# Kernel optimization log

Hardware: AMD Instinct MI355X
Metric: run time of the kernel (lower is better)

Reference implementation:

```python
import jax, jax.numpy as jnp
import numpy as np

CNN_DIM = 256
CLASS_NUM = 6
NHOPS = 2
ATT_DIM = 50


def conv1d(x, w, b, pad):
    # x: [B, Cin, L], w: [Cout, Cin, K]
    y = jax.lax.conv_general_dilated(x, w, (1,), [(pad, pad)],
                                     dimension_numbers=('NCH', 'OIH', 'NCH'))
    return y + b[None, :, None]


def setup_inputs() -> dict:
    key = jax.random.key(0)
    ks = jax.random.split(key, 16)
    B, L, V, GE, DE = 8, 128, 30000, 300, 100
    IN = GE + DE
    C = CLASS_NUM
    s = 0.02
    inp = {}
    inp['x'] = jax.random.randint(ks[0], (B, L), 0, V)
    inp['x_len'] = L  # python int, stands in for x_len[0] (max length)
    inp['x_mask'] = jnp.ones((B, L), dtype=jnp.float32)
    inp['gen_table'] = jax.random.normal(ks[1], (V, GE), jnp.float32) * s
    inp['domain_table'] = jax.random.normal(ks[2], (V, DE), jnp.float32) * s
    inp['w1'] = jax.random.normal(ks[3], (128, IN, 5)) * s
    inp['b1'] = jnp.zeros((128,))
    inp['w2'] = jax.random.normal(ks[4], (128, IN, 3)) * s
    inp['b2'] = jnp.zeros((128,))
    inp['w3'] = jax.random.normal(ks[5], (256, 256, 5)) * s
    inp['b3'] = jnp.zeros((256,))
    inp['w4'] = jax.random.normal(ks[6], (256, 256, 5)) * s
    inp['b4'] = jnp.zeros((256,))
    inp['w5'] = jax.random.normal(ks[7], (256, 256, 5)) * s
    inp['b5'] = jnp.zeros((256,))
    inp['wq'] = jax.random.normal(ks[8], (CNN_DIM, ATT_DIM)) * s
    inp['bq'] = jnp.zeros((ATT_DIM,))
    inp['wv'] = jax.random.normal(ks[9], (CNN_DIM, ATT_DIM)) * s
    inp['bv'] = jnp.zeros((ATT_DIM,))
    inp['vv'] = jax.random.normal(ks[10], (ATT_DIM,)) * s
    inp['wf'] = jax.random.normal(ks[11], (2 * CNN_DIM + 3 * C, 2 * CNN_DIM)) * s
    inp['bf'] = jnp.zeros((2 * CNN_DIM,))
    inp['wc'] = jax.random.normal(ks[12], (2 * CNN_DIM, C)) * s
    inp['bc'] = jnp.zeros((C,))
    return inp


def reference(x, x_len, x_mask, gen_table, domain_table,
              w1, b1, w2, b2, w3, b3, w4, b4, w5, b5,
              wq, bq, wv, bv, vv, wf, bf, wc, bc):
    # embeddings (dropout omitted: eval mode)
    emb = jnp.concatenate([gen_table[x], domain_table[x]], axis=2)  # [B,L,400]
    xe = jnp.swapaxes(emb, 1, 2)  # [B,400,L]
    xc = jax.nn.relu(jnp.concatenate([conv1d(xe, w1, b1, 2),
                                      conv1d(xe, w2, b2, 1)], axis=1))
    xc = jax.nn.relu(conv1d(xc, w3, b3, 2))
    xc = jax.nn.relu(conv1d(xc, w4, b4, 2))
    xc = jax.nn.relu(conv1d(xc, w5, b5, 2))
    xc = jnp.swapaxes(xc, 1, 2)[:, :x_len, :]  # [B,L,256]
    mask = x_mask[:, :x_len]
    # perceptron (additive) self-attention: v^T tanh(Wq q_i + Wv v_j)
    q = xc @ wq + bq  # [B,L,50]
    v = xc @ wv + bv  # [B,L,50]
    scores = jnp.tanh(q[:, :, None, :] + v[:, None, :, :]) @ vv  # [B,L,L]
    scores = jnp.where(mask[:, None, :] == 0, -1e9, scores)
    attn = jax.nn.softmax(scores, axis=2)
    merged = jnp.einsum('bij,bjd->bid', attn, xc) * mask[:, :, None]
    xc = xc + merged
    B, L, D = xc.shape
    # grid features: (i,j) -> [h_i, h_j]
    features = jnp.concatenate([
        jnp.broadcast_to(xc[:, :, None, :], (B, L, L, D)),
        jnp.broadcast_to(xc[:, None, :, :], (B, L, L, D))], axis=3)  # [B,L,L,512]
    # upper-triangular validity mask on the grid
    m2 = jnp.triu(mask[:, None, :] * mask[:, :, None])[..., None]  # [B,L,L,1]
    logits = features @ wc + bc  # [B,L,L,C]
    for _ in range(NHOPS):
        probs = logits
        lg = probs * m2
        lm = jnp.maximum(jnp.max(lg, axis=1), jnp.max(lg, axis=2))  # [B,L,C]
        row = jnp.broadcast_to(lm[:, :, None, :], (B, L, L, lm.shape[-1]))
        grid = jnp.concatenate([row, jnp.swapaxes(row, 1, 2)], axis=3)  # [B,L,L,2C]
        features = jnp.concatenate([features, grid, probs], axis=3) @ wf + bf
        logits = features @ wc + bc
    return logits
```

## Files before the change

### kernel.cpp

```cpp
#include <hip/hip_runtime.h>
#include <math.h>

#define LSEQ 128
#define BB 8
#define M_TOK (BB*LSEQ)

typedef __attribute__((ext_vector_type(8))) short short8;
typedef __attribute__((ext_vector_type(4))) float floatx4;

__device__ __forceinline__ unsigned short bf16_rne(float v) {
    union { float f; unsigned u; } a; a.f = v;
    return (unsigned short)((a.u + 0x7fffu + ((a.u >> 16) & 1u)) >> 16);
}
__device__ __forceinline__ float bf16_to_f(unsigned short h) {
    union { unsigned u; float f; } b; b.u = ((unsigned)h) << 16;
    return b.f;
}
__device__ __forceinline__ void split2(float v, unsigned short& h, unsigned short& l) {
    h = bf16_rne(v);
    l = bf16_rne(v - bf16_to_f(h));
}

struct PreArgs {
    const float *w1, *w2, *w3, *w4, *w5;
    unsigned short *B1h, *B1l, *B2h, *B2l, *B3h, *B3l, *B4h, *B4l, *B5h, *B5l;
    const int* x;
    const float* gen;
    const float* dom;
    unsigned short *Eh, *El;
    const float* wf;
    const float* wc;
    float* Wfc;
};
__global__ __launch_bounds__(256) void stage_kernel(PreArgs a) {
    int y = blockIdx.y;
    int tid = threadIdx.x;
    if (y < 3) {
        const float* w = (y == 0) ? a.w3 : (y == 1) ? a.w4 : a.w5;
        unsigned short* dh = (y == 0) ? a.B3h : (y == 1) ? a.B4h : a.B5h;
        unsigned short* dl = (y == 0) ? a.B3l : (y == 1) ? a.B4l : a.B5l;
        int idx = blockIdx.x * 256 + tid;
        int j = idx & 7;
        int n = (idx >> 3) & 255;
        int g = idx >> 11;
        int cg = g & 31, kk = g >> 5;
        int ci = cg * 8 + j;
        float v = w[(n * 256 + ci) * 5 + kk];
        unsigned short h, l; split2(v, h, l);
        dh[idx] = h; dl[idx] = l;
    } else if (y == 3) {
        int idx = blockIdx.x * 256 + tid;
        if (idx >= 5 * 52 * 128 * 8) return;
        int j = idx & 7;
        int n = (idx >> 3) & 127;
        int g = idx >> 10;
        int cg = g % 52, kk = g / 52;
        int ci = cg * 8 + j;
        float v = (ci < 400) ? a.w1[(n * 400 + ci) * 5 + kk] : 0.f;
        unsigned short h, l; split2(v, h, l);
        a.B1h[idx] = h; a.B1l[idx] = l;
    } else if (y == 4) {
        int idx = blockIdx.x * 256 + tid;
        if (idx >= 3 * 52 * 128 * 8) return;
        int j = idx & 7;
        int n = (idx >> 3) & 127;
        int g = idx >> 10;
        int cg = g % 52, kk = g / 52;
        int ci = cg * 8 + j;
        float v = (ci < 400) ? a.w2[(n * 400 + ci) * 3 + kk] : 0.f;
        unsigned short h, l; split2(v, h, l);
        a.B2h[idx] = h; a.B2l[idx] = l;
    } else if (y == 5) {
        int m = blockIdx.x;
        if (m >= M_TOK) return;
        int t = a.x[m];
        for (int c = tid; c < 416; c += 256) {
            float v = (c < 300) ? a.gen[t * 300 + c]
                    : (c < 400) ? a.dom[t * 100 + (c - 300)] : 0.f;
            unsigned short h, l; split2(v, h, l);
            a.Eh[m * 416 + c] = h;
            a.El[m * 416 + c] = l;
        }
    } else {
        int r = blockIdx.x;
        if (r >= 512 || tid >= 64) return;
        int l = tid;
        float p[6] = {0,0,0,0,0,0};
        const float* row = a.wf + r * 512;
        #pragma unroll
        for (int k = 0; k < 8; ++k) {
            int n = l + 64 * k;
            float v = row[n];
            #pragma unroll
            for (int c = 0; c < 6; ++c) p[c] += v * a.wc[n * 6 + c];
        }
        #pragma unroll
        for (int c = 0; c < 6; ++c)
            for (int off = 32; off >= 1; off >>= 1) p[c] += __shfl_xor(p[c], off, 64);
        if (l == 0) {
            #pragma unroll
            for (int c = 0; c < 6; ++c) a.Wfc[r * 6 + c] = p[c];
        }
    }
}

__global__ __launch_bounds__(256) void conv1_mfma(
        const unsigned short* __restrict__ Eh, const unsigned short* __restrict__ El,
        const unsigned short* __restrict__ B1h, const unsigned short* __restrict__ B1l,
        const unsigned short* __restrict__ B2h, const unsigned short* __restrict__ B2l,
        const float* __restrict__ b1, const float* __restrict__ b2,
        unsigned short* __restrict__ Xoh, unsigned short* __restrict__ Xol,
        const float* __restrict__ wf, const float* __restrict__ bf,
        const float* __restrict__ wc, const float* __restrict__ Wfc,
        float* __restrict__ U) {
    __shared__ __align__(16) unsigned short xsh[20 * 424];
    __shared__ __align__(16) unsigned short xsl[20 * 424];
    int by = blockIdx.y;
    int tid = threadIdx.x;
    if (by == 4) {
        if (tid >= 64) return;
        int l = tid;
        for (int i = 0; i < 9; ++i) {
            int r = blockIdx.x + 64 * i;
            if (r >= 531) break;
            const float* row = (r < 530) ? (wf + r * 512) : bf;
            float p[12];
            #pragma unroll
            for (int c = 0; c < 12; ++c) p[c] = 0.f;
            #pragma unroll
            for (int k = 0; k < 8; ++k) {
                int n = l + 64 * k;
                float v = row[n];
                #pragma unroll
                for (int c = 0; c < 6; ++c) {
                    p[c]     += v * wc[n * 6 + c];
                    p[c + 6] += v * Wfc[n * 6 + c];
                }
            }
            #pragma unroll
            for (int c = 0; c < 12; ++c)
                for (int off = 32; off >= 1; off >>= 1) p[c] += __shfl_xor(p[c], off, 64);
            if (l == 0) {
                #pragma unroll
                for (int c = 0; c < 12; ++c) U[r * 12 + c] = p[c];
            }
        }
        return;
    }
    int mt = blockIdx.x;
    int p0 = mt * 16;
    int b = p0 >> 7, l0 = p0 & 127;
    for (int i = tid; i < 2 * 1040; i += 256) {
        int sel = i >= 1040;
        int u2 = sel ? i - 1040 : i;
        int j = u2 / 52, cg = u2 % 52;
        int l = l0 - 2 + j;
        short8 v = {0,0,0,0,0,0,0,0};
        if (l >= 0 && l < 128) {
            const unsigned short* src = (sel ? El : Eh) + (b * 128 + l) * 416 + cg * 8;
            v = *(const short8*)src;
        }
        *(short8*)((sel ? xsl : xsh) + j * 424 + cg * 8) = v;
    }
    __syncthreads();
    int w = tid >> 6, lane = tid & 63;
    int m = lane & 15, q = lane >> 4;
    bool br2 = (by >= 2);
    int n0b = (by & 1) * 64;
    int nB = n0b + w * 16 + m;
    floatx4 acc0 = {0,0,0,0}, acc1 = {0,0,0,0}, acc2 = {0,0,0,0};
    if (!br2) {
        for (int kk = 0; kk < 5; ++kk) {
            const unsigned short* arh = xsh + (m + kk) * 424;
            const unsigned short* arl = xsl + (m + kk) * 424;
            #pragma unroll
            for (int u = 0; u < 13; ++u) {
                short8 ah = *(const short8*)(arh + u * 32 + q * 8);
                short8 al = *(const short8*)(arl + u * 32 + q * 8);
                int boff = (((kk * 52 + u * 4 + q) * 128) + nB) * 8;
                short8 bh = *(const short8*)(B1h + boff);
                short8 bl = *(const short8*)(B1l + boff);
                acc0 = __builtin_amdgcn_mfma_f32_16x16x32_bf16(ah, bh, acc0, 0, 0, 0);
                acc1 = __builtin_amdgcn_mfma_f32_16x16x32_bf16(ah, bl, acc1, 0, 0, 0);
                acc2 = __builtin_amdgcn_mfma_f32_16x16x32_bf16(al, bh, acc2, 0, 0, 0);
            }
        }
    } else {
        for (int kk = 0; kk < 3; ++kk) {
            const unsigned short* arh = xsh + (m + kk + 1) * 424;
            const unsigned short* arl = xsl + (m + kk + 1) * 424;
            #pragma unroll
            for (int u = 0; u < 13; ++u) {
                short8 ah = *(const short8*)(arh + u * 32 + q * 8);
                short8 al = *(const short8*)(arl + u * 32 + q * 8);
                int boff = (((kk * 52 + u * 4 + q) * 128) + nB) * 8;
                short8 bh = *(const short8*)(B2h + boff);
                short8 bl = *(const short8*)(B2l + boff);
                acc0 = __builtin_amdgcn_mfma_f32_16x16x32_bf16(ah, bh, acc0, 0, 0, 0);
                acc1 = __builtin_amdgcn_mfma_f32_16x16x32_bf16(ah, bl, acc1, 0, 0, 0);
                acc2 = __builtin_amdgcn_mfma_f32_16x16x32_bf16(al, bh, acc2, 0, 0, 0);
            }
        }
    }
    __syncthreads();
    float* fl = (float*)xsh;
    #pragma unroll
    for (int reg = 0; reg < 4; ++reg)
        fl[(q * 4 + reg) * 68 + w * 16 + m] = acc0[reg] + acc1[reg] + acc2[reg];
    __syncthreads();
    int ocb = br2 ? 128 + n0b : n0b;
    const float* bias = br2 ? b2 : b1;
    #pragma unroll
    for (int i = 0; i < 4; ++i) {
        int e = tid + 256 * i;
        int mm = e >> 6, nn = e & 63;
        float val = fl[mm * 68 + nn] + bias[n0b + nn];
        val = fmaxf(val, 0.f);
        unsigned short h, l; split2(val, h, l);
        int o = (p0 + mm) * 256 + ocb + nn;
        Xoh[o] = h; Xol[o] = l;
    }
}

__global__ __launch_bounds__(256) void conv256_mfma(
        const unsigned short* __restrict__ Xih, const unsigned short* __restrict__ Xil,
        const unsigned short* __restrict__ Bh, const unsigned short* __restrict__ Bl,
        const float* __restrict__ bias, int outmode,
        unsigned short* __restrict__ Xoh, unsigned short* __restrict__ Xol,
        float* __restrict__ fout) {
    __shared__ __align__(16) unsigned short xsh[36 * 264];
    __shared__ __align__(16) unsigned short xsl[36 * 264];
    int mt = blockIdx.x;
    int p0 = mt * 32;
    int b = p0 >> 7, l0 = p0 & 127;
    int n0 = blockIdx.y * 64;
    int tid = threadIdx.x;
    for (int i = tid; i < 2 * 1152; i += 256) {
        int sel = i >= 1152;
        int u2 = sel ? i - 1152 : i;
        int j = u2 >> 5, cg = u2 & 31;
        int l = l0 - 2 + j;
        short8 v = {0,0,0,0,0,0,0,0};
        if (l >= 0 && l < 128) {
            const unsigned short* src = (sel ? Xil : Xih) + (b * 128 + l) * 256 + cg * 8;
            v = *(const short8*)src;
        }
        *(short8*)((sel ? xsl : xsh) + j * 264 + cg * 8) = v;
    }
    __syncthreads();
    int w = tid >> 6, lane = tid & 63;
    int m = lane & 15, q = lane >> 4;
    int nB = n0 + w * 16 + m;
    floatx4 acc0a = {0,0,0,0}, acc1a = {0,0,0,0}, acc2a = {0,0,0,0};
    floatx4 acc0b = {0,0,0,0}, acc1b = {0,0,0,0}, acc2b = {0,0,0,0};
    for (int kk = 0; kk < 5; ++kk) {
        const unsigned short* arh0 = xsh + (m + kk) * 264;
        const unsigned short* arl0 = xsl + (m + kk) * 264;
        const unsigned short* arh1 = arh0 + 16 * 264;
        const unsigned short* arl1 = arl0 + 16 * 264;
        #pragma unroll
        for (int u = 0; u < 8; ++u) {
            short8 ah0 = *(const short8*)(arh0 + u * 32 + q * 8);
            short8 al0 = *(const short8*)(arl0 + u * 32 + q * 8);
            short8 ah1 = *(const short8*)(arh1 + u * 32 + q * 8);
            short8 al1 = *(const short8*)(arl1 + u * 32 + q * 8);
            int boff = (((kk * 32 + u * 4 + q) * 256) + nB) * 8;
            short8 bh = *(const short8*)(Bh + boff);
            short8 bl = *(const short8*)(Bl + boff);
            acc0a = __builtin_amdgcn_mfma_f32_16x16x32_bf16(ah0, bh, acc0a, 0, 0, 0);
            acc1a = __builtin_amdgcn_mfma_f32_16x16x32_bf16(ah0, bl, acc1a, 0, 0, 0);
            acc2a = __builtin_amdgcn_mfma_f32_16x16x32_bf16(al0, bh, acc2a, 0, 0, 0);
            acc0b = __builtin_amdgcn_mfma_f32_16x16x32_bf16(ah1, bh, acc0b, 0, 0, 0);
            acc1b = __builtin_amdgcn_mfma_f32_16x16x32_bf16(ah1, bl, acc1b, 0, 0, 0);
            acc2b = __builtin_amdgcn_mfma_f32_16x16x32_bf16(al1, bh, acc2b, 0, 0, 0);
        }
    }
    __syncthreads();
    float* fl = (float*)xsh;
    #pragma unroll
    for (int reg = 0; reg < 4; ++reg) {
        fl[(q * 4 + reg) * 68 + w * 16 + m]        = acc0a[reg] + acc1a[reg] + acc2a[reg];
        fl[(16 + q * 4 + reg) * 68 + w * 16 + m]   = acc0b[reg] + acc1b[reg] + acc2b[reg];
    }
    __syncthreads();
    #pragma unroll
    for (int i = 0; i < 8; ++i) {
        int e = tid + 256 * i;
        int mm = e >> 6, nn = e & 63;
        float val = fl[mm * 68 + nn] + bias[n0 + nn];
        val = fmaxf(val, 0.f);
        int o = (p0 + mm) * 256 + n0 + nn;
        if (outmode == 0) {
            unsigned short h, l; split2(val, h, l);
            Xoh[o] = h; Xol[o] = l;
        } else {
            fout[o] = val;
        }
    }
}

__global__ __launch_bounds__(128) void qv_v2(const float* __restrict__ xc,
        const float* __restrict__ wq, const float* __restrict__ bq,
        const float* __restrict__ wv, const float* __restrict__ bv,
        float* __restrict__ q, float* __restrict__ v) {
    int m = blockIdx.x;
    int tid = threadIdx.x;
    int w = tid >> 6, d = tid & 63;
    if (d >= 50) return;
    const float* W = w ? wv : wq;
    float a = w ? bv[d] : bq[d];
    const float* xm = xc + m * 256;
    #pragma unroll 8
    for (int c = 0; c < 256; ++c) a += xm[c] * W[c * 50 + d];
    (w ? v : q)[m * 50 + d] = a;
}

__global__ __launch_bounds__(256) void attn_v2(const float* __restrict__ xc,
        const float* __restrict__ q, const float* __restrict__ v,
        const float* __restrict__ vv, const float* __restrict__ xmask,
        const float* __restrict__ wc, const float* __restrict__ bc,
        float* __restrict__ xc2, float* __restrict__ f0, float* __restrict__ g0) {
    __shared__ float vs[128 * 50];
    __shared__ float spart[128], aarr[128], xrow[256], qrow[52], vvs[52], red[4];
    int bi = blockIdx.x;
    int b = bi >> 7;
    int tid = threadIdx.x;
    for (int idx = tid; idx < 128 * 50; idx += 256) vs[idx] = v[b * 6400 + idx];
    if (tid < 50) { qrow[tid] = q[bi * 50 + tid]; vvs[tid] = vv[tid]; }
    __syncthreads();
    int j = tid & 127, half = tid >> 7;
    int d0 = half * 25;
    const float* vj = vs + j * 50 + d0;
    float s = 0.f;
    #pragma unroll
    for (int d = 0; d < 25; ++d) {
        float x = qrow[d0 + d] + vj[d];
        float e = __expf(2.f * x);
        s += (1.f - 2.f / (e + 1.f)) * vvs[d0 + d];
    }
    if (half) spart[j] = s;
    __syncthreads();
    float stot = 0.f;
    if (!half) {
        stot = s + spart[j];
        if (xmask[b * LSEQ + j] == 0.f) stot = -1e9f;
    }
    if (tid < 128) {
        float m = stot;
        #pragma unroll
        for (int off = 32; off >= 1; off >>= 1) m = fmaxf(m, __shfl_xor(m, off, 64));
        if ((tid & 63) == 0) red[tid >> 6] = m;
    }
    __syncthreads();
    float mx = fmaxf(red[0], red[1]);
    float e = 0.f;
    if (tid < 128) {
        e = __expf(stot - mx);
        float su = e;
        #pragma unroll
        for (int off = 32; off >= 1; off >>= 1) su += __shfl_xor(su, off, 64);
        if ((tid & 63) == 0) red[2 + (tid >> 6)] = su;
    }
    __syncthreads();
    float denom = red[2] + red[3];
    if (tid < 128) aarr[j] = e / denom;
    __syncthreads();
    float maskI = xmask[bi];
    const float* xcb = xc + b * LSEQ * 256;
    float acc = 0.f;
    #pragma unroll 8
    for (int jj = 0; jj < 128; ++jj) acc += aarr[jj] * xcb[jj * 256 + tid];
    float val = xc[bi * 256 + tid] + acc * maskI;
    xc2[bi * 256 + tid] = val;
    xrow[tid] = val;
    __syncthreads();
    int grp = tid >> 4, l16 = tid & 15;
    if (grp < 12) {
        int c = grp % 6, gsel = grp / 6;
        const float* wcc = wc + gsel * 256 * 6 + c;
        float a = 0.f;
        #pragma unroll
        for (int ch = l16; ch < 256; ch += 16) a += xrow[ch] * wcc[ch * 6];
        #pragma unroll
        for (int off = 8; off >= 1; off >>= 1) a += __shfl_down(a, off, 16);
        if (l16 == 0) {
            if (gsel == 0) f0[bi * 6 + c] = a + bc[c];
            else           g0[bi * 6 + c] = a;
        }
    }
}

__global__ __launch_bounds__(256) void hop1_kernel(const float* __restrict__ xc2,
        const float* __restrict__ U, const float* __restrict__ f0,
        const float* __restrict__ g0, const float* __restrict__ bc,
        float* __restrict__ outF, float* __restrict__ outG) {
    __shared__ float sf0[768], sg0[768], sfw[768], sgw[768], lms[768];
    int b = blockIdx.x >> 4, grp = blockIdx.x & 15;
    int tid = threadIdx.x;
    for (int i = tid; i < 768; i += 256) {
        sf0[i] = f0[b * 768 + i];
        sg0[i] = g0[b * 768 + i];
    }
    __syncthreads();
    int p = tid;
    float fv[6], gv[6], pf[6], sx[6];
    if (p < 128) {
        #pragma unroll
        for (int c = 0; c < 6; ++c) {
            fv[c] = sf0[p * 6 + c]; gv[c] = sg0[p * 6 + c];
            pf[c] = fv[c]; sx[c] = gv[c];
            sfw[p * 6 + c] = fv[c]; sgw[p * 6 + c] = gv[c];
        }
    }
    __syncthreads();
    #pragma unroll
    for (int off = 1; off < 128; off <<= 1) {
        float av[6], dv[6];
        if (p < 128) {
            #pragma unroll
            for (int c = 0; c < 6; ++c) {
                av[c] = (p >= off) ? sfw[(p - off) * 6 + c] : -INFINITY;
                dv[c] = (p + off < 128) ? sgw[(p + off) * 6 + c] : -INFINITY;
            }
        }
        __syncthreads();
        if (p < 128) {
            #pragma unroll
            for (int c = 0; c < 6; ++c) {
                pf[c] = fmaxf(pf[c], av[c]); sx[c] = fmaxf(sx[c], dv[c]);
                sfw[p * 6 + c] = pf[c]; sgw[p * 6 + c] = sx[c];
            }
        }
        __syncthreads();
    }
    if (p < 128) {
        #pragma unroll
        for (int c = 0; c < 6; ++c) {
            float M1 = pf[c] + gv[c];
            if (p < LSEQ - 1) M1 = fmaxf(M1, 0.f);
            float M2 = fv[c] + sx[c];
            if (p > 0) M2 = fmaxf(M2, 0.f);
            lms[p * 6 + c] = fmaxf(M1, M2);
        }
    }
    __syncthreads();
    int t = tid >> 5, lane = tid & 31;
    int ptok = grp * 8 + t;
    int m = b * 128 + ptok;
    float p24[24];
    #pragma unroll
    for (int c = 0; c < 24; ++c) p24[c] = 0.f;
    const floatx4* U4 = (const floatx4*)U;
    const float* xm = xc2 + m * 256;
    #pragma unroll
    for (int kk = 0; kk < 8; ++kk) {
        int k = lane + 32 * kk;
        float a = xm[k];
        floatx4 u0[3], u1[3];
        #pragma unroll
        for (int t3 = 0; t3 < 3; ++t3) { u0[t3] = U4[k * 3 + t3]; u1[t3] = U4[(256 + k) * 3 + t3]; }
        #pragma unroll
        for (int t3 = 0; t3 < 3; ++t3)
            #pragma unroll
            for (int qd = 0; qd < 4; ++qd) {
                p24[t3 * 4 + qd]      += a * u0[t3][qd];
                p24[12 + t3 * 4 + qd] += a * u1[t3][qd];
            }
    }
    #pragma unroll
    for (int c = 0; c < 24; ++c)
        for (int off = 16; off >= 1; off >>= 1) p24[c] += __shfl_xor(p24[c], off, 32);
    if (lane < 12) {
        int c = lane;
        float s0 = p24[c], s1 = p24[12 + c];
        #pragma unroll
        for (int jj = 0; jj < 6; ++jj) {
            float lmv = lms[ptok * 6 + jj];
            float f0v = sf0[ptok * 6 + jj];
            float g0v = sg0[ptok * 6 + jj];
            float dbv = U[(524 + jj) * 12 + c];
            s0 += lmv * U[(512 + jj) * 12 + c] + f0v * dbv;
            s1 += lmv * U[(518 + jj) * 12 + c] + g0v * dbv;
        }
        s0 += U[530 * 12 + c];
        if (c < 6) s0 += bc[c];
        outF[m * 12 + c] = s0;
        outG[m * 12 + c] = s1;
    }
}

__global__ __launch_bounds__(256) void hop2_kernel(const float* __restrict__ f1phi,
        const float* __restrict__ g1gam, const float* __restrict__ U,
        const float* __restrict__ bc, float* __restrict__ out) {
    __shared__ float f1s[128 * 12], g1s[128 * 12];
    __shared__ float sfw[768], sgw[768], lm1s[768], f2s[768], g2s[768];
    __shared__ float Us[228], bcs[6];
    int b = blockIdx.x >> 4, ys = blockIdx.x & 15;
    int tid = threadIdx.x;
    for (int i = tid; i < 1536; i += 256) {
        f1s[i] = f1phi[b * 1536 + i];
        g1s[i] = g1gam[b * 1536 + i];
    }
    if (tid < 228) Us[tid] = U[512 * 12 + tid];
    if (tid < 6) bcs[tid] = bc[tid];
    __syncthreads();
    int p = tid;
    float fv[6], gv[6], pf[6], sx[6];
    if (p < 128) {
        #pragma unroll
        for (int c = 0; c < 6; ++c) {
            fv[c] = f1s[p * 12 + c]; gv[c] = g1s[p * 12 + c];
            pf[c] = fv[c]; sx[c] = gv[c];
            sfw[p * 6 + c] = fv[c]; sgw[p * 6 + c] = gv[c];
        }
    }
    __syncthreads();
    #pragma unroll
    for (int off = 1; off < 128; off <<= 1) {
        float av[6], dv[6];
        if (p < 128) {
            #pragma unroll
            for (int c = 0; c < 6; ++c) {
                av[c] = (p >= off) ? sfw[(p - off) * 6 + c] : -INFINITY;
                dv[c] = (p + off < 128) ? sgw[(p + off) * 6 + c] : -INFINITY;
            }
        }
        __syncthreads();
        if (p < 128) {
            #pragma unroll
            for (int c = 0; c < 6; ++c) {
                pf[c] = fmaxf(pf[c], av[c]); sx[c] = fmaxf(sx[c], dv[c]);
                sfw[p * 6 + c] = pf[c]; sgw[p * 6 + c] = sx[c];
            }
        }
        __syncthreads();
    }
    if (p < 128) {
        #pragma unroll
        for (int c = 0; c < 6; ++c) {
            float M1 = pf[c] + gv[c];
            if (p < LSEQ - 1) M1 = fmaxf(M1, 0.f);
            float M2 = fv[c] + sx[c];
            if (p > 0) M2 = fmaxf(M2, 0.f);
            lm1s[p * 6 + c] = fmaxf(M1, M2);
        }
    }
    __syncthreads();
    if (p < 128) {
        float lmv[6], f1v[6], g1v[6];
        #pragma unroll
        for (int jj = 0; jj < 6; ++jj) {
            lmv[jj] = lm1s[p * 6 + jj];
            f1v[jj] = f1s[p * 12 + jj];
            g1v[jj] = g1s[p * 12 + jj];
        }
        #pragma unroll
        for (int c = 0; c < 6; ++c) {
            float sf = f1s[p * 12 + 6 + c] + Us[18 * 12 + c] + bcs[c];
            float sg = g1s[p * 12 + 6 + c];
            #pragma unroll
            for (int jj = 0; jj < 6; ++jj) {
                sf += lmv[jj] * Us[jj * 12 + c]       + f1v[jj] * Us[(12 + jj) * 12 + c];
                sg += lmv[jj] * Us[(6 + jj) * 12 + c] + g1v[jj] * Us[(12 + jj) * 12 + c];
            }
            f2s[p * 6 + c] = sf;
            g2s[p * 6 + c] = sg;
        }
    }
    __syncthreads();
    floatx4* out4 = (floatx4*)out;
    for (int e = tid; e < 1536; e += 256) {
        int i = e / 12, part = e - i * 12;
        floatx4 wv;
        #pragma unroll
        for (int qd = 0; qd < 4; ++qd) {
            int idx = part * 4 + qd;
            int jj = idx / 6, c = idx - jj * 6;
            wv[qd] = f2s[i * 6 + c] + g2s[(ys * 8 + jj) * 6 + c];
        }
        out4[(b * 128 + i) * 192 + ys * 12 + part] = wv;
    }
}

extern "C" void kernel_launch(void* const* d_in, const int* in_sizes, int n_in,
                              void* d_out, int out_size, void* d_ws, size_t ws_size,
                              hipStream_t stream) {
    const int*   x     = (const int*)d_in[0];
    const float* xmask = (const float*)d_in[2];
    const float* gen   = (const float*)d_in[3];
    const float* dom   = (const float*)d_in[4];
    const float* w1    = (const float*)d_in[5];
    const float* b1    = (const float*)d_in[6];
    const float* w2    = (const float*)d_in[7];
    const float* b2    = (const float*)d_in[8];
    const float* w3    = (const float*)d_in[9];
    const float* b3    = (const float*)d_in[10];
    const float* w4    = (const float*)d_in[11];
    const float* b4    = (const float*)d_in[12];
    const float* w5    = (const float*)d_in[13];
    const float* b5    = (const float*)d_in[14];
    const float* wq    = (const float*)d_in[15];
    const float* bq    = (const float*)d_in[16];
    const float* wv    = (const float*)d_in[17];
    const float* bv    = (const float*)d_in[18];
    const float* vv    = (const float*)d_in[19];
    const float* wf    = (const float*)d_in[20];
    const float* bf    = (const float*)d_in[21];
    const float* wc    = (const float*)d_in[22];
    const float* bc    = (const float*)d_in[23];

    float* fb = (float*)d_ws;
    float* bufB  = fb;
    float* xc2   = bufB  + 262144;
    float* qb    = xc2   + 262144;
    float* vb    = qb    + 51200;
    float* Wfc   = vb    + 51200;
    float* U     = Wfc   + 3072;
    float* f0    = U     + 6376;
    float* g0    = f0    + 6144;
    float* lm0   = g0    + 6144;
    float* lm1   = lm0   + 6144;
    float* f1phi = lm1   + 6144;
    float* g1gam = f1phi + 12288;
    float* f2    = g1gam + 12288;
    float* g2    = f2    + 6144;
    (void)lm0; (void)lm1; (void)f2;
    unsigned short* sb = (unsigned short*)(g2 + 6144 + 32);
    unsigned short* Eh  = sb;             sb += 425984;
    unsigned short* El  = sb;             sb += 425984;
    unsigned short* B1h = sb;             sb += 266240;
    unsigned short* B1l = sb;             sb += 266240;
    unsigned short* B2h = sb;             sb += 159744;
    unsigned short* B2l = sb;             sb += 159744;
    unsigned short* B3h = sb;             sb += 327680;
    unsigned short* B3l = sb;             sb += 327680;
    unsigned short* B4h = sb;             sb += 327680;
    unsigned short* B4l = sb;             sb += 327680;
    unsigned short* B5h = sb;             sb += 327680;
    unsigned short* B5l = sb;             sb += 327680;
    unsigned short* X3h = sb;             sb += 262144;
    unsigned short* X3l = sb;             sb += 262144;
    unsigned short* X4h = sb;             sb += 262144;
    unsigned short* X4l = sb;             sb += 262144;

    PreArgs pa;
    pa.w1 = w1; pa.w2 = w2; pa.w3 = w3; pa.w4 = w4; pa.w5 = w5;
    pa.B1h = B1h; pa.B1l = B1l; pa.B2h = B2h; pa.B2l = B2l;
    pa.B3h = B3h; pa.B3l = B3l; pa.B4h = B4h; pa.B4l = B4l;
    pa.B5h = B5h; pa.B5l = B5l;
    pa.x = x; pa.gen = gen; pa.dom = dom; pa.Eh = Eh; pa.El = El;
    pa.wf = wf; pa.wc = wc; pa.Wfc = Wfc;
    stage_kernel<<<dim3(1280, 7), 256, 0, stream>>>(pa);

    conv1_mfma<<<dim3(64, 5), 256, 0, stream>>>(Eh, El, B1h, B1l, B2h, B2l, b1, b2,
                                                X3h, X3l, wf, bf, wc, Wfc, U);
    conv256_mfma<<<dim3(32, 4), 256, 0, stream>>>(X3h, X3l, B3h, B3l, b3, 0,
                                                  X4h, X4l, nullptr);
    conv256_mfma<<<dim3(32, 4), 256, 0, stream>>>(X4h, X4l, B4h, B4l, b4, 0,
                                                  X3h, X3l, nullptr);
    conv256_mfma<<<dim3(32, 4), 256, 0, stream>>>(X3h, X3l, B5h, B5l, b5, 1,
                                                  nullptr, nullptr, bufB);

    qv_v2<<<M_TOK, 128, 0, stream>>>(bufB, wq, bq, wv, bv, qb, vb);
    attn_v2<<<M_TOK, 256, 0, stream>>>(bufB, qb, vb, vv, xmask, wc, bc, xc2, f0, g0);

    hop1_kernel<<<128, 256, 0, stream>>>(xc2, U, f0, g0, bc, f1phi, g1gam);
    hop2_kernel<<<128, 256, 0, stream>>>(f1phi, g1gam, U, bc, (float*)d_out);
}
```

Before: 254.9 us.

## Fuse conv layers and q/v projection into one persistent kernel with grid barriers

Merges conv1, the three 256-channel convs and the q/v projection into a single persistent kernel of 320 blocks that synchronise through atomic grid barriers, replacing five separate launches. The conv256 tile shrinks from 32 to 16 rows so 256 blocks cover each layer, which raises parallelism but halves B-operand reuse per block. Barrier counters are zeroed inside stage_kernel. The barriers rely on all 320 blocks being co-resident, and idle blocks spin at every barrier.

```diff
diff --git a/kernel.cpp b/kernel.cpp
--- a/kernel.cpp
+++ b/kernel.cpp
@@ -4,6 +4,7 @@
 #define LSEQ 128
 #define BB 8
 #define M_TOK (BB*LSEQ)
+#define CONV_BLOCKS 320
 
 typedef __attribute__((ext_vector_type(8))) short short8;
 typedef __attribute__((ext_vector_type(4))) float floatx4;
@@ -19,6 +20,18 @@
 __device__ __forceinline__ void split2(float v, unsigned short& h, unsigned short& l) {
     h = bf16_rne(v);
     l = bf16_rne(v - bf16_to_f(h));
+}
+
+__device__ __forceinline__ void gbar(int* bars, int phase, int nb) {
+    __syncthreads();
+    if (threadIdx.x == 0) {
+        __threadfence();
+        __hip_atomic_fetch_add(bars + phase * 64, 1, __ATOMIC_ACQ_REL, __HIP_MEMORY_SCOPE_AGENT);
+        while (__hip_atomic_load(bars + phase * 64, __ATOMIC_ACQUIRE, __HIP_MEMORY_SCOPE_AGENT) < nb)
+            __builtin_amdgcn_s_sleep(2);
+        __threadfence();
+    }
+    __syncthreads();
 }
 
 struct PreArgs {
@@ -31,6 +44,7 @@
     const float* wf;
     const float* wc;
     float* Wfc;
+    int* bars;
 };
 __global__ __launch_bounds__(256) void stage_kernel(PreArgs a) {
     int y = blockIdx.y;
@@ -82,8 +96,12 @@
             a.El[m * 416 + c] = l;
         }
     } else {
+        if (blockIdx.x >= 512) {
+            if (blockIdx.x == 512) a.bars[tid] = 0;
+            return;
+        }
+        if (tid >= 64) return;
         int r = blockIdx.x;
-        if (r >= 512 || tid >= 64) return;
         int l = tid;
         float p[6] = {0,0,0,0,0,0};
         const float* row = a.wf + r * 512;
@@ -104,140 +122,18 @@
     }
 }
 
-__global__ __launch_bounds__(256) void conv1_mfma(
-        const unsigned short* __restrict__ Eh, const unsigned short* __restrict__ El,
-        const unsigned short* __restrict__ B1h, const unsigned short* __restrict__ B1l,
-        const unsigned short* __restrict__ B2h, const unsigned short* __restrict__ B2l,
-        const float* __restrict__ b1, const float* __restrict__ b2,
-        unsigned short* __restrict__ Xoh, unsigned short* __restrict__ Xol,
-        const float* __restrict__ wf, const float* __restrict__ bf,
-        const float* __restrict__ wc, const float* __restrict__ Wfc,
-        float* __restrict__ U) {
-    __shared__ __align__(16) unsigned short xsh[20 * 424];
-    __shared__ __align__(16) unsigned short xsl[20 * 424];
-    int by = blockIdx.y;
-    int tid = threadIdx.x;
-    if (by == 4) {
-        if (tid >= 64) return;
-        int l = tid;
-        for (int i = 0; i < 9; ++i) {
-            int r = blockIdx.x + 64 * i;
-            if (r >= 531) break;
-            const float* row = (r < 530) ? (wf + r * 512) : bf;
-            float p[12];
-            #pragma unroll
-            for (int c = 0; c < 12; ++c) p[c] = 0.f;
-            #pragma unroll
-            for (int k = 0; k < 8; ++k) {
-                int n = l + 64 * k;
-                float v = row[n];
-                #pragma unroll
-                for (int c = 0; c < 6; ++c) {
-                    p[c]     += v * wc[n * 6 + c];
-                    p[c + 6] += v * Wfc[n * 6 + c];
-                }
-            }
-            #pragma unroll
-            for (int c = 0; c < 12; ++c)
-                for (int off = 32; off >= 1; off >>= 1) p[c] += __shfl_xor(p[c], off, 64);
-            if (l == 0) {
-                #pragma unroll
-                for (int c = 0; c < 12; ++c) U[r * 12 + c] = p[c];
-            }
-        }
-        return;
-    }
-    int mt = blockIdx.x;
-    int p0 = mt * 16;
-    int b = p0 >> 7, l0 = p0 & 127;
-    for (int i = tid; i < 2 * 1040; i += 256) {
-        int sel = i >= 1040;
-        int u2 = sel ? i - 1040 : i;
-        int j = u2 / 52, cg = u2 % 52;
-        int l = l0 - 2 + j;
-        short8 v = {0,0,0,0,0,0,0,0};
-        if (l >= 0 && l < 128) {
-            const unsigned short* src = (sel ? El : Eh) + (b * 128 + l) * 416 + cg * 8;
-            v = *(const short8*)src;
-        }
-        *(short8*)((sel ? xsl : xsh) + j * 424 + cg * 8) = v;
-    }
-    __syncthreads();
-    int w = tid >> 6, lane = tid & 63;
-    int m = lane & 15, q = lane >> 4;
-    bool br2 = (by >= 2);
-    int n0b = (by & 1) * 64;
-    int nB = n0b + w * 16 + m;
-    floatx4 acc0 = {0,0,0,0}, acc1 = {0,0,0,0}, acc2 = {0,0,0,0};
-    if (!br2) {
-        for (int kk = 0; kk < 5; ++kk) {
-            const unsigned short* arh = xsh + (m + kk) * 424;
-            const unsigned short* arl = xsl + (m + kk) * 424;
-            #pragma unroll
-            for (int u = 0; u < 13; ++u) {
-                short8 ah = *(const short8*)(arh + u * 32 + q * 8);
-                short8 al = *(const short8*)(arl + u * 32 + q * 8);
-                int boff = (((kk * 52 + u * 4 + q) * 128) + nB) * 8;
-                short8 bh = *(const short8*)(B1h + boff);
-                short8 bl = *(const short8*)(B1l + boff);
-                acc0 = __builtin_amdgcn_mfma_f32_16x16x32_bf16(ah, bh, acc0, 0, 0, 0);
-                acc1 = __builtin_amdgcn_mfma_f32_16x16x32_bf16(ah, bl, acc1, 0, 0, 0);
-                acc2 = __builtin_amdgcn_mfma_f32_16x16x32_bf16(al, bh, acc2, 0, 0, 0);
-            }
-        }
-    } else {
-        for (int kk = 0; kk < 3; ++kk) {
-            const unsigned short* arh = xsh + (m + kk + 1) * 424;
-            const unsigned short* arl = xsl + (m + kk + 1) * 424;
-            #pragma unroll
-            for (int u = 0; u < 13; ++u) {
-                short8 ah = *(const short8*)(arh + u * 32 + q * 8);
-                short8 al = *(const short8*)(arl + u * 32 + q * 8);
-                int boff = (((kk * 52 + u * 4 + q) * 128) + nB) * 8;
-                short8 bh = *(const short8*)(B2h + boff);
-                short8 bl = *(const short8*)(B2l + boff);
-                acc0 = __builtin_amdgcn_mfma_f32_16x16x32_bf16(ah, bh, acc0, 0, 0, 0);
-                acc1 = __builtin_amdgcn_mfma_f32_16x16x32_bf16(ah, bl, acc1, 0, 0, 0);
-                acc2 = __builtin_amdgcn_mfma_f32_16x16x32_bf16(al, bh, acc2, 0, 0, 0);
-            }
-        }
-    }
-    __syncthreads();
-    float* fl = (float*)xsh;
-    #pragma unroll
-    for (int reg = 0; reg < 4; ++reg)
-        fl[(q * 4 + reg) * 68 + w * 16 + m] = acc0[reg] + acc1[reg] + acc2[reg];
-    __syncthreads();
-    int ocb = br2 ? 128 + n0b : n0b;
-    const float* bias = br2 ? b2 : b1;
-    #pragma unroll
-    for (int i = 0; i < 4; ++i) {
-        int e = tid + 256 * i;
-        int mm = e >> 6, nn = e & 63;
-        float val = fl[mm * 68 + nn] + bias[n0b + nn];
-        val = fmaxf(val, 0.f);
-        unsigned short h, l; split2(val, h, l);
-        int o = (p0 + mm) * 256 + ocb + nn;
-        Xoh[o] = h; Xol[o] = l;
-    }
-}
-
-__global__ __launch_bounds__(256) void conv256_mfma(
+__device__ void conv256_body(int mt, int n0, int tid,
         const unsigned short* __restrict__ Xih, const unsigned short* __restrict__ Xil,
         const unsigned short* __restrict__ Bh, const unsigned short* __restrict__ Bl,
         const float* __restrict__ bias, int outmode,
         unsigned short* __restrict__ Xoh, unsigned short* __restrict__ Xol,
-        float* __restrict__ fout) {
-    __shared__ __align__(16) unsigned short xsh[36 * 264];
-    __shared__ __align__(16) unsigned short xsl[36 * 264];
-    int mt = blockIdx.x;
-    int p0 = mt * 32;
+        float* __restrict__ fout,
+        unsigned short* xsh, unsigned short* xsl) {
+    int p0 = mt * 16;
     int b = p0 >> 7, l0 = p0 & 127;
-    int n0 = blockIdx.y * 64;
-    int tid = threadIdx.x;
-    for (int i = tid; i < 2 * 1152; i += 256) {
-        int sel = i >= 1152;
-        int u2 = sel ? i - 1152 : i;
+    for (int i = tid; i < 2 * 640; i += 256) {
+        int sel = i >= 640;
+        int u2 = sel ? i - 640 : i;
         int j = u2 >> 5, cg = u2 & 31;
         int l = l0 - 2 + j;
         short8 v = {0,0,0,0,0,0,0,0};
@@ -251,40 +147,30 @@
     int w = tid >> 6, lane = tid & 63;
     int m = lane & 15, q = lane >> 4;
     int nB = n0 + w * 16 + m;
-    floatx4 acc0a = {0,0,0,0}, acc1a = {0,0,0,0}, acc2a = {0,0,0,0};
-    floatx4 acc0b = {0,0,0,0}, acc1b = {0,0,0,0}, acc2b = {0,0,0,0};
+    floatx4 acc0 = {0,0,0,0}, acc1 = {0,0,0,0}, acc2 = {0,0,0,0};
     for (int kk = 0; kk < 5; ++kk) {
-        const unsigned short* arh0 = xsh + (m + kk) * 264;
-        const unsigned short* arl0 = xsl + (m + kk) * 264;
-        const unsigned short* arh1 = arh0 + 16 * 264;
-        const unsigned short* arl1 = arl0 + 16 * 264;
+        const unsigned short* arh = xsh + (m + kk) * 264;
+        const unsigned short* arl = xsl + (m + kk) * 264;
         #pragma unroll
         for (int u = 0; u < 8; ++u) {
-            short8 ah0 = *(const short8*)(arh0 + u * 32 + q * 8);
-            short8 al0 = *(const short8*)(arl0 + u * 32 + q * 8);
-            short8 ah1 = *(const short8*)(arh1 + u * 32 + q * 8);
-            short8 al1 = *(const short8*)(arl1 + u * 32 + q * 8);
+            short8 ah = *(const short8*)(arh + u * 32 + q * 8);
+            short8 al = *(const short8*)(arl + u * 32 + q * 8);
             int boff = (((kk * 32 + u * 4 + q) * 256) + nB) * 8;
             short8 bh = *(const short8*)(Bh + boff);
             short8 bl = *(const short8*)(Bl + boff);
-            acc0a = __builtin_amdgcn_mfma_f32_16x16x32_bf16(ah0, bh, acc0a, 0, 0, 0);
-            acc1a = __builtin_amdgcn_mfma_f32_16x16x32_bf16(ah0, bl, acc1a, 0, 0, 0);
-            acc2a = __builtin_amdgcn_mfma_f32_16x16x32_bf16(al0, bh, acc2a, 0, 0, 0);
-            acc0b = __builtin_amdgcn_mfma_f32_16x16x32_bf16(ah1, bh, acc0b, 0, 0, 0);
-            acc1b = __builtin_amdgcn_mfma_f32_16x16x32_bf16(ah1, bl, acc1b, 0, 0, 0);
-            acc2b = __builtin_amdgcn_mfma_f32_16x16x32_bf16(al1, bh, acc2b, 0, 0, 0);
+            acc0 = __builtin_amdgcn_mfma_f32_16x16x32_bf16(ah, bh, acc0, 0, 0, 0);
+            acc1 = __builtin_amdgcn_mfma_f32_16x16x32_bf16(ah, bl, acc1, 0, 0, 0);
+            acc2 = __builtin_amdgcn_mfma_f32_16x16x32_bf16(al, bh, acc2, 0, 0, 0);
         }
     }
     __syncthreads();
     float* fl = (float*)xsh;
     #pragma unroll
-    for (int reg = 0; reg < 4; ++reg) {
-        fl[(q * 4 + reg) * 68 + w * 16 + m]        = acc0a[reg] + acc1a[reg] + acc2a[reg];
-        fl[(16 + q * 4 + reg) * 68 + w * 16 + m]   = acc0b[reg] + acc1b[reg] + acc2b[reg];
-    }
-    __syncthreads();
-    #pragma unroll
-    for (int i = 0; i < 8; ++i) {
+    for (int reg = 0; reg < 4; ++reg)
+        fl[(q * 4 + reg) * 68 + w * 16 + m] = acc0[reg] + acc1[reg] + acc2[reg];
+    __syncthreads();
+    #pragma unroll
+    for (int i = 0; i < 4; ++i) {
         int e = tid + 256 * i;
         int mm = e >> 6, nn = e & 63;
         float val = fl[mm * 68 + nn] + bias[n0 + nn];
@@ -297,22 +183,164 @@
             fout[o] = val;
         }
     }
-}
-
-__global__ __launch_bounds__(128) void qv_v2(const float* __restrict__ xc,
-        const float* __restrict__ wq, const float* __restrict__ bq,
-        const float* __restrict__ wv, const float* __restrict__ bv,
-        float* __restrict__ q, float* __restrict__ v) {
-    int m = blockIdx.x;
+    __syncthreads();
+}
+
+struct ConvArgs {
+    const unsigned short *Eh, *El, *B1h, *B1l, *B2h, *B2l;
+    const unsigned short *B3h, *B3l, *B4h, *B4l, *B5h, *B5l;
+    unsigned short *X3h, *X3l, *X4h, *X4l;
+    const float *b1, *b2, *b3, *b4, *b5;
+    const float *wf, *bf, *wc, *Wfc;
+    float *U;
+    float *bufB;
+    const float *wq, *bq, *wv, *bv;
+    float *qb, *vb;
+    int *bars;
+};
+__global__ __launch_bounds__(256, 2) void conv_all(ConvArgs a) {
+    __shared__ __align__(16) unsigned short xsh[20 * 424];
+    __shared__ __align__(16) unsigned short xsl[20 * 424];
+    int bid = blockIdx.x;
     int tid = threadIdx.x;
-    int w = tid >> 6, d = tid & 63;
-    if (d >= 50) return;
-    const float* W = w ? wv : wq;
-    float a = w ? bv[d] : bq[d];
-    const float* xm = xc + m * 256;
-    #pragma unroll 8
-    for (int c = 0; c < 256; ++c) a += xm[c] * W[c * 50 + d];
-    (w ? v : q)[m * 50 + d] = a;
+    int by = bid >> 6, mt = bid & 63;
+
+    if (by == 4) {
+        if (tid < 64) {
+            int l = tid;
+            for (int i = 0; i < 9; ++i) {
+                int r = mt + 64 * i;
+                if (r >= 531) break;
+                const float* row = (r < 530) ? (a.wf + r * 512) : a.bf;
+                float p[12];
+                #pragma unroll
+                for (int c = 0; c < 12; ++c) p[c] = 0.f;
+                #pragma unroll
+                for (int k = 0; k < 8; ++k) {
+                    int n = l + 64 * k;
+                    float v = row[n];
+                    #pragma unroll
+                    for (int c = 0; c < 6; ++c) {
+                        p[c]     += v * a.wc[n * 6 + c];
+                        p[c + 6] += v * a.Wfc[n * 6 + c];
+                    }
+                }
+                #pragma unroll
+                for (int c = 0; c < 12; ++c)
+                    for (int off = 32; off >= 1; off >>= 1) p[c] += __shfl_xor(p[c], off, 64);
+                if (l == 0) {
+                    #pragma unroll
+                    for (int c = 0; c < 12; ++c) a.U[r * 12 + c] = p[c];
+                }
+            }
+        }
+    } else {
+        int p0 = mt * 16;
+        int b = p0 >> 7, l0 = p0 & 127;
+        for (int i = tid; i < 2 * 1040; i += 256) {
+            int sel = i >= 1040;
+            int u2 = sel ? i - 1040 : i;
+            int j = u2 / 52, cg = u2 % 52;
+            int l = l0 - 2 + j;
+            short8 v = {0,0,0,0,0,0,0,0};
+            if (l >= 0 && l < 128) {
+                const unsigned short* src = (sel ? a.El : a.Eh) + (b * 128 + l) * 416 + cg * 8;
+                v = *(const short8*)src;
+            }
+            *(short8*)((sel ? xsl : xsh) + j * 424 + cg * 8) = v;
+        }
+        __syncthreads();
+        int w = tid >> 6, lane = tid & 63;
+        int m = lane & 15, q = lane >> 4;
+        bool br2 = (by >= 2);
+        int n0b = (by & 1) * 64;
+        int nB = n0b + w * 16 + m;
+        floatx4 acc0 = {0,0,0,0}, acc1 = {0,0,0,0}, acc2 = {0,0,0,0};
+        if (!br2) {
+            for (int kk = 0; kk < 5; ++kk) {
+                const unsigned short* arh = xsh + (m + kk) * 424;
+                const unsigned short* arl = xsl + (m + kk) * 424;
+                #pragma unroll
+                for (int u = 0; u < 13; ++u) {
+                    short8 ah = *(const short8*)(arh + u * 32 + q * 8);
+                    short8 al = *(const short8*)(arl + u * 32 + q * 8);
+                    int boff = (((kk * 52 + u * 4 + q) * 128) + nB) * 8;
+                    short8 bh = *(const short8*)(a.B1h + boff);
+                    short8 bl = *(const short8*)(a.B1l + boff);
+                    acc0 = __builtin_amdgcn_mfma_f32_16x16x32_bf16(ah, bh, acc0, 0, 0, 0);
+                    acc1 = __builtin_amdgcn_mfma_f32_16x16x32_bf16(ah, bl, acc1, 0, 0, 0);
+                    acc2 = __builtin_amdgcn_mfma_f32_16x16x32_bf16(al, bh, acc2, 0, 0, 0);
+                }
+            }
+        } else {
+            for (int kk = 0; kk < 3; ++kk) {
+                const unsigned short* arh = xsh + (m + kk + 1) * 424;
+                const unsigned short* arl = xsl + (m + kk + 1) * 424;
+                #pragma unroll
+                for (int u = 0; u < 13; ++u) {
+                    short8 ah = *(const short8*)(arh + u * 32 + q * 8);
+                    short8 al = *(const short8*)(arl + u * 32 + q * 8);
+                    int boff = (((kk * 52 + u * 4 + q) * 128) + nB) * 8;
+                    short8 bh = *(const short8*)(a.B2h + boff);
+                    short8 bl = *(const short8*)(a.B2l + boff);
+                    acc0 = __builtin_amdgcn_mfma_f32_16x16x32_bf16(ah, bh, acc0, 0, 0, 0);
+                    acc1 = __builtin_amdgcn_mfma_f32_16x16x32_bf16(ah, bl, acc1, 0, 0, 0);
+                    acc2 = __builtin_amdgcn_mfma_f32_16x16x32_bf16(al, bh, acc2, 0, 0, 0);
+                }
+            }
+        }
+        __syncthreads();
+        float* fl = (float*)xsh;
+        #pragma unroll
+        for (int reg = 0; reg < 4; ++reg)
+            fl[(q * 4 + reg) * 68 + w * 16 + m] = acc0[reg] + acc1[reg] + acc2[reg];
+        __syncthreads();
+        int ocb = br2 ? 128 + n0b : n0b;
+        const float* bias = br2 ? a.b2 : a.b1;
+        #pragma unroll
+        for (int i = 0; i < 4; ++i) {
+            int e = tid + 256 * i;
+            int mm = e >> 6, nn = e & 63;
+            float val = fl[mm * 68 + nn] + bias[n0b + nn];
+            val = fmaxf(val, 0.f);
+            unsigned short h, l; split2(val, h, l);
+            int o = (p0 + mm) * 256 + ocb + nn;
+            a.X3h[o] = h; a.X3l[o] = l;
+        }
+        __syncthreads();
+    }
+    gbar(a.bars, 0, CONV_BLOCKS);
+
+    if (bid < 256)
+        conv256_body(bid & 63, (bid >> 6) * 64, tid, a.X3h, a.X3l, a.B3h, a.B3l,
+                     a.b3, 0, a.X4h, a.X4l, nullptr, xsh, xsl);
+    gbar(a.bars, 1, CONV_BLOCKS);
+
+    if (bid < 256)
+        conv256_body(bid & 63, (bid >> 6) * 64, tid, a.X4h, a.X4l, a.B4h, a.B4l,
+                     a.b4, 0, a.X3h, a.X3l, nullptr, xsh, xsl);
+    gbar(a.bars, 2, CONV_BLOCKS);
+
+    if (bid < 256)
+        conv256_body(bid & 63, (bid >> 6) * 64, tid, a.X3h, a.X3l, a.B5h, a.B5l,
+                     a.b5, 1, nullptr, nullptr, a.bufB, xsh, xsl);
+    gbar(a.bars, 3, CONV_BLOCKS);
+
+    #pragma unroll
+    for (int k = 0; k < 2; ++k) {
+        int item = bid * 256 + tid + CONV_BLOCKS * 256 * k;
+        if (item >= 131072) break;
+        int m = item >> 7, r = item & 127;
+        int w = r >> 6, d = r & 63;
+        if (d < 50) {
+            const float* W = w ? a.wv : a.wq;
+            float acc = w ? a.bv[d] : a.bq[d];
+            const float* xm = a.bufB + m * 256;
+            #pragma unroll 8
+            for (int c = 0; c < 256; ++c) acc += xm[c] * W[c * 50 + d];
+            (w ? a.vb : a.qb)[m * 50 + d] = acc;
+        }
+    }
 }
 
 __global__ __launch_bounds__(256) void attn_v2(const float* __restrict__ xc,
@@ -624,7 +652,8 @@
     float* g1gam = f1phi + 12288;
     float* f2    = g1gam + 12288;
     float* g2    = f2    + 6144;
-    (void)lm0; (void)lm1; (void)f2;
+    int* bars = (int*)lm0;
+    (void)lm1; (void)f2;
     unsigned short* sb = (unsigned short*)(g2 + 6144 + 32);
     unsigned short* Eh  = sb;             sb += 425984;
     unsigned short* El  = sb;             sb += 425984;
@@ -649,19 +678,19 @@
     pa.B3h = B3h; pa.B3l = B3l; pa.B4h = B4h; pa.B4l = B4l;
     pa.B5h = B5h; pa.B5l = B5l;
     pa.x = x; pa.gen = gen; pa.dom = dom; pa.Eh = Eh; pa.El = El;
-    pa.wf = wf; pa.wc = wc; pa.Wfc = Wfc;
+    pa.wf = wf; pa.wc = wc; pa.Wfc = Wfc; pa.bars = bars;
     stage_kernel<<<dim3(1280, 7), 256, 0, stream>>>(pa);
 
-    conv1_mfma<<<dim3(64, 5), 256, 0, stream>>>(Eh, El, B1h, B1l, B2h, B2l, b1, b2,
-                                                X3h, X3l, wf, bf, wc, Wfc, U);
-    conv256_mfma<<<dim3(32, 4), 256, 0, stream>>>(X3h, X3l, B3h, B3l, b3, 0,
-                                                  X4h, X4l, nullptr);
-    conv256_mfma<<<dim3(32, 4), 256, 0, stream>>>(X4h, X4l, B4h, B4l, b4, 0,
-                                                  X3h, X3l, nullptr);
-    conv256_mfma<<<dim3(32, 4), 256, 0, stream>>>(X3h, X3l, B5h, B5l, b5, 1,
-                                                  nullptr, nullptr, bufB);
-
-    qv_v2<<<M_TOK, 128, 0, stream>>>(bufB, wq, bq, wv, bv, qb, vb);
+    ConvArgs ca;
+    ca.Eh = Eh; ca.El = El; ca.B1h = B1h; ca.B1l = B1l; ca.B2h = B2h; ca.B2l = B2l;
+    ca.B3h = B3h; ca.B3l = B3l; ca.B4h = B4h; ca.B4l = B4l; ca.B5h = B5h; ca.B5l = B5l;
+    ca.X3h = X3h; ca.X3l = X3l; ca.X4h = X4h; ca.X4l = X4l;
+    ca.b1 = b1; ca.b2 = b2; ca.b3 = b3; ca.b4 = b4; ca.b5 = b5;
+    ca.wf = wf; ca.bf = bf; ca.wc = wc; ca.Wfc = Wfc; ca.U = U; ca.bufB = bufB;
+    ca.wq = wq; ca.bq = bq; ca.wv = wv; ca.bv = bv; ca.qb = qb; ca.vb = vb;
+    ca.bars = bars;
+    conv_all<<<CONV_BLOCKS, 256, 0, stream>>>(ca);
+
     attn_v2<<<M_TOK, 256, 0, stream>>>(bufB, qb, vb, vv, xmask, wc, bc, xc2, f0, g0);
 
     hop1_kernel<<<128, 256, 0, stream>>>(xc2, U, f0, g0, bc, f1phi, g1gam);
```

After: 455.0 us. 1.79x slower.
